# Optimization experiments

Measured on AMD Instinct MI355X. Metric: run time of the kernel, lower is better.

The kernel has to match this reference:

```python
import jax, jax.numpy as jnp
import numpy as np

B, T, D, H = 2, 2048, 1024, 16
HD = D // H  # head_dim = 64


def setup_inputs() -> dict:
    key = jax.random.key(0)
    ks = jax.random.split(key, 6)
    x = jax.random.normal(ks[0], (B, T, D), dtype=jnp.float32)
    wq = jax.random.normal(ks[1], (D, D), dtype=jnp.float32) * (D ** -0.5)
    wk = jax.random.normal(ks[2], (D, D), dtype=jnp.float32) * (D ** -0.5)
    wv = jax.random.normal(ks[3], (D, D), dtype=jnp.float32) * (D ** -0.5)
    wo = jax.random.normal(ks[4], (D, D), dtype=jnp.float32) * (D ** -0.5)
    # RoPE tables: standard inverse-frequency angles, shape [T, head_dim]
    inv_freq = 1.0 / (10000.0 ** (jnp.arange(0, HD, 2, dtype=jnp.float32) / HD))
    ang = jnp.arange(T, dtype=jnp.float32)[:, None] * inv_freq[None, :]  # [T, HD/2]
    ang = jnp.concatenate([ang, ang], axis=-1)  # [T, HD]
    cos, sin = jnp.cos(ang), jnp.sin(ang)
    # causal mask [1,1,T,T]: True where attention is allowed
    mask = jnp.tril(jnp.ones((T, T), dtype=bool))[None, None]
    return {"x": x, "wq": wq, "wk": wk, "wv": wv, "wo": wo,
            "cos": cos, "sin": sin, "mask": mask}


def rotate_half(u):
    u1, u2 = jnp.split(u, 2, axis=-1)
    return jnp.concatenate([-u2, u1], axis=-1)


def reference(x, wq, wk, wv, wo, cos, sin, mask):
    b, t, c = x.shape
    # projections (nn.Linear: y = x @ W^T), reshape to [B, H, T, HD]
    def proj(w):
        return (x @ w.T).reshape(b, t, H, HD).transpose(0, 2, 1, 3)
    q, k, v = proj(wq), proj(wk), proj(wv)
    # inline RoPE: cos/sin broadcast [1,1,T,HD]
    co = cos[:t][None, None]
    si = sin[:t][None, None]
    q = q * co + rotate_half(q) * si
    k = k * co + rotate_half(k) * si
    # scaled dot-product attention with causal mask
    att = jnp.einsum("bhqd,bhkd->bhqk", q, k) * (HD ** -0.5)
    att = jnp.where(mask[:, :, :t, :t], att, -jnp.inf)
    att = jax.nn.softmax(att, axis=-1)
    out = jnp.einsum("bhqk,bhkd->bhqd", att, v)
    out = out.transpose(0, 2, 1, 3).reshape(b, t, c)
    return out @ wo.T
```

## Files before the change

### kernel.cpp

```cpp
#include <hip/hip_runtime.h>
#include <hip/hip_bf16.h>
#include <type_traits>

#define B_  2
#define T_  2048
#define D_  1024
#define H_  16
#define HD_ 64

typedef __attribute__((ext_vector_type(8))) short bf16x8;
typedef __attribute__((ext_vector_type(4))) float f32x4;

__device__ __forceinline__ unsigned short f2b(float x) {
  union { __hip_bfloat16 h; unsigned short u; } c;
  c.h = __float2bfloat16(x);
  return c.u;
}
__device__ __forceinline__ float b2f(unsigned short u) {
  union { unsigned short u; __hip_bfloat16 h; } c;
  c.u = u;
  return __bfloat162float(c.h);
}

__device__ __forceinline__ void ld_g2l_16(const unsigned short* g, unsigned short* l) {
  auto gp = (const __attribute__((address_space(1))) unsigned int*)g;
  auto lp = (__attribute__((address_space(3))) unsigned int*)l;
  __builtin_amdgcn_global_load_lds(gp, lp, 16, 0, 0);
}

__global__ void __launch_bounds__(256)
cast_all(const float* __restrict__ x, const float* __restrict__ wq,
         const float* __restrict__ wk, const float* __restrict__ wv,
         const float* __restrict__ wo, unsigned short* __restrict__ xb,
         unsigned short* __restrict__ wp) {
  int blk = blockIdx.x;
  const float* src;
  unsigned short* dst;
  size_t off;
  if (blk < 2048) {
    src = x; dst = xb; off = (size_t)blk * 2048;
  } else {
    int t = (blk - 2048) >> 9;
    int r = (blk - 2048) & 511;
    src = (t == 0) ? wq : (t == 1) ? wk : (t == 2) ? wv : wo;
    dst = wp + (size_t)t * 1048576;
    off = (size_t)r * 2048;
  }
  size_t i = off + threadIdx.x * 8;
  float4 a = *(const float4*)(src + i);
  float4 b = *(const float4*)(src + i + 4);
  unsigned short h[8] = {f2b(a.x), f2b(a.y), f2b(a.z), f2b(a.w),
                         f2b(b.x), f2b(b.y), f2b(b.z), f2b(b.w)};
  *(uint4*)(dst + i) = *(uint4*)h;
}

template <typename OutT, int MROWS>
__device__ __forceinline__ void gemm_core(const unsigned short* __restrict__ A,
                                          const unsigned short* __restrict__ Bw,
                                          OutT* __restrict__ C, int K, int Ldc) {
  constexpr int MT = MROWS / 32;
  __shared__ unsigned short a_s[MROWS * 32];
  __shared__ unsigned short b_s[128 * 32];
  const int tid = threadIdx.x;
  const int lane = tid & 63;
  const int w = tid >> 6;
  const int m16 = lane & 15;
  const int quad = lane >> 4;
  const int wm = w >> 1, wn = w & 1;
  const int rl = lane >> 2;
  const int cl = (lane & 3) * 8;

  f32x4 acc[MT][4];
#pragma unroll
  for (int i = 0; i < MT; i++)
#pragma unroll
    for (int j = 0; j < 4; j++) acc[i][j] = (f32x4){0.f, 0.f, 0.f, 0.f};

  for (int k0 = 0; k0 < K; k0 += 32) {
#pragma unroll
    for (int t = 0; t < MROWS / 64; t++) {
      int seg = w * 16 + t * 64;
      ld_g2l_16(A + (size_t)(seg + rl) * K + k0 + cl, &a_s[seg * 32]);
    }
#pragma unroll
    for (int j = 0; j < 2; j++) {
      int seg = w * 32 + j * 16;
      ld_g2l_16(Bw + (size_t)(seg + rl) * K + k0 + cl, &b_s[seg * 32]);
    }
    __syncthreads();
    bf16x8 af[MT], bfr[4];
#pragma unroll
    for (int mt = 0; mt < MT; mt++)
      af[mt] = *(const bf16x8*)&a_s[(wm * (MT * 16) + mt * 16 + m16) * 32 + quad * 8];
#pragma unroll
    for (int nt = 0; nt < 4; nt++)
      bfr[nt] = *(const bf16x8*)&b_s[(wn * 64 + nt * 16 + m16) * 32 + quad * 8];
#pragma unroll
    for (int mt = 0; mt < MT; mt++)
#pragma unroll
      for (int nt = 0; nt < 4; nt++)
        acc[mt][nt] = __builtin_amdgcn_mfma_f32_16x16x32_bf16(af[mt], bfr[nt], acc[mt][nt], 0, 0, 0);
    __syncthreads();
  }
#pragma unroll
  for (int mt = 0; mt < MT; mt++)
#pragma unroll
    for (int nt = 0; nt < 4; nt++)
#pragma unroll
      for (int reg = 0; reg < 4; reg++) {
        OutT* p = C + (size_t)(wm * (MT * 16) + mt * 16 + quad * 4 + reg) * Ldc + wn * 64 + nt * 16 + m16;
        if constexpr (std::is_same_v<OutT, float>) *p = acc[mt][nt][reg];
        else *p = f2b(acc[mt][nt][reg]);
      }
}

__global__ void __launch_bounds__(256)
gemm_qkv(const unsigned short* __restrict__ xb, const unsigned short* __restrict__ wp,
         unsigned short* __restrict__ qkv) {
  const int nb = blockIdx.x;
  const int bm = blockIdx.y * 128;
  const int mi = nb >> 3;
  const int bn = (nb & 7) * 128;
  gemm_core<unsigned short, 128>(xb + (size_t)bm * D_,
                                 wp + (size_t)(mi * 1024 + bn) * D_,
                                 qkv + (size_t)mi * (4096ull * D_) + (size_t)bm * D_ + bn,
                                 D_, D_);
}

__global__ void __launch_bounds__(256)
gemm_out(const unsigned short* __restrict__ Ab, const unsigned short* __restrict__ wob,
         float* __restrict__ C) {
  const int bn = blockIdx.x * 128;
  const int bm = blockIdx.y * 64;
  gemm_core<float, 64>(Ab + (size_t)bm * D_, wob + (size_t)bn * D_,
                       C + (size_t)bm * D_ + bn, D_, D_);
}

__global__ void __launch_bounds__(256)
rope_kernel(unsigned short* __restrict__ Q, unsigned short* __restrict__ Kp,
            const float* __restrict__ cosT, const float* __restrict__ sinT) {
  int i = blockIdx.x * 256 + threadIdx.x;
  int d = i & (HD_ - 1);
  int t = (i >> 10) & (T_ - 1);
  float c = cosT[t * HD_ + d];
  float s = sinT[t * HD_ + d];
  float q = b2f(Q[i]), k = b2f(Kp[i]);
  float qp = __shfl_xor(q, 32, 64);
  float kp = __shfl_xor(k, 32, 64);
  float sgn = (d < 32) ? -1.f : 1.f;
  Q[i] = f2b(fmaf(sgn * qp, s, q * c) * 0.125f);
  Kp[i] = f2b(fmaf(sgn * kp, s, k * c));
}

__global__ void __launch_bounds__(512, 4)
attn_kernel(const unsigned short* __restrict__ Q, const unsigned short* __restrict__ K,
            const unsigned short* __restrict__ V, unsigned short* __restrict__ O) {
  __shared__ __align__(16) unsigned short qp_s[128][72];
  __shared__ __align__(16) unsigned short k_s[64][72];
  __shared__ __align__(16) unsigned short vt_s[64][72];

  const int tid = threadIdx.x;
  const int lane = tid & 63;
  const int w = tid >> 6;
  const int m16 = lane & 15;
  const int quad = lane >> 4;

  int x = blockIdx.x;
  int bh, qb;
  if (x < 256) { bh = x >> 4; qb = x & 15; }
  else         { bh = 16 + ((x - 256) >> 4); qb = 15 - ((x - 256) & 15); }
  const int b = bh >> 4, h = bh & 15;
  const int q0 = qb * 128;

  const unsigned short* Qb = Q + ((size_t)b * T_ + q0) * D_ + h * HD_;
  const unsigned short* Kb = K + (size_t)b * T_ * D_ + h * HD_;
  const unsigned short* Vb = V + (size_t)b * T_ * D_ + h * HD_;

#pragma unroll
  for (int i = 0; i < 2; i++) {
    int idx = tid + i * 512;
    int r = idx >> 3, c = idx & 7;
    *(bf16x8*)&qp_s[r][c * 8] = *(const bf16x8*)(Qb + (size_t)r * D_ + c * 8);
  }
  __syncthreads();
  bf16x8 q_frag[2];
  q_frag[0] = *(const bf16x8*)&qp_s[w * 16 + m16][quad * 8];
  q_frag[1] = *(const bf16x8*)&qp_s[w * 16 + m16][32 + quad * 8];

  f32x4 o_acc[4];
#pragma unroll
  for (int dt = 0; dt < 4; dt++) o_acc[dt] = (f32x4){0.f, 0.f, 0.f, 0.f};
  float m_i = -1e30f, l_i = 0.f;
  const int rg = q0 + w * 16 + m16;
  const int rmax = q0 + w * 16 + 15;
  const int ktmax = (q0 + 127) >> 6;

  for (int kt = 0; kt <= ktmax; kt++) {
    {
      int r = tid >> 3, c = tid & 7;
      const unsigned short* Kt = Kb + (size_t)(kt * 64 + r) * D_ + c * 8;
      const unsigned short* Vt = Vb + (size_t)(kt * 64 + r) * D_ + c * 8;
      *(bf16x8*)&k_s[r][c * 8] = *(const bf16x8*)Kt;
      bf16x8 vv = *(const bf16x8*)Vt;
      int jb = r >> 3, jl = r & 7;
#pragma unroll
      for (int e = 0; e < 8; e++) {
        int d = c * 8 + e;
        vt_s[d][((jb ^ (d >> 3)) << 3) | jl] = ((const unsigned short*)&vv)[e];
      }
    }
    __syncthreads();

    if (kt * 64 <= rmax) {
      f32x4 sf[4];
#pragma unroll
      for (int jt = 0; jt < 4; jt++) {
        bf16x8 a0 = *(const bf16x8*)&k_s[jt * 16 + m16][quad * 8];
        bf16x8 a1 = *(const bf16x8*)&k_s[jt * 16 + m16][32 + quad * 8];
        f32x4 acc = (f32x4){0.f, 0.f, 0.f, 0.f};
        acc = __builtin_amdgcn_mfma_f32_16x16x32_bf16(a0, q_frag[0], acc, 0, 0, 0);
        acc = __builtin_amdgcn_mfma_f32_16x16x32_bf16(a1, q_frag[1], acc, 0, 0, 0);
        sf[jt] = acc;
      }
      if (kt * 64 + 63 > q0 + w * 16) {
#pragma unroll
        for (int jt = 0; jt < 4; jt++)
#pragma unroll
          for (int reg = 0; reg < 4; reg++) {
            int jg = kt * 64 + jt * 16 + quad * 4 + reg;
            if (jg > rg) sf[jt][reg] = -1e30f;
          }
      }
      float mx = sf[0][0];
#pragma unroll
      for (int jt = 0; jt < 4; jt++)
#pragma unroll
        for (int reg = 0; reg < 4; reg++) mx = fmaxf(mx, sf[jt][reg]);
      mx = fmaxf(mx, __shfl_xor(mx, 16, 64));
      mx = fmaxf(mx, __shfl_xor(mx, 32, 64));
      float mn = fmaxf(m_i, mx);
      float alpha = __expf(m_i - mn);
      float lt = 0.f;
      float p[4][4];
#pragma unroll
      for (int jt = 0; jt < 4; jt++)
#pragma unroll
        for (int reg = 0; reg < 4; reg++) {
          p[jt][reg] = __expf(sf[jt][reg] - mn);
          lt += p[jt][reg];
        }
      lt += __shfl_xor(lt, 16, 64);
      lt += __shfl_xor(lt, 32, 64);
      l_i = l_i * alpha + lt;
      m_i = mn;
#pragma unroll
      for (int dt = 0; dt < 4; dt++)
#pragma unroll
        for (int reg = 0; reg < 4; reg++) o_acc[dt][reg] *= alpha;
#pragma unroll
      for (int jt = 0; jt < 4; jt++) {
        unsigned short pk[4] = {f2b(p[jt][0]), f2b(p[jt][1]), f2b(p[jt][2]), f2b(p[jt][3])};
        *(uint2*)&qp_s[w * 16 + m16][jt * 16 + quad * 4] = *(uint2*)pk;
      }
      bf16x8 bp0 = *(const bf16x8*)&qp_s[w * 16 + m16][quad * 8];
      bf16x8 bp1 = *(const bf16x8*)&qp_s[w * 16 + m16][32 + quad * 8];
#pragma unroll
      for (int dt = 0; dt < 4; dt++) {
        int rowd = dt * 16 + m16;
        bf16x8 a0 = *(const bf16x8*)&vt_s[rowd][((quad ^ (rowd >> 3)) << 3)];
        bf16x8 a1 = *(const bf16x8*)&vt_s[rowd][(((4 + quad) ^ (rowd >> 3)) << 3)];
        o_acc[dt] = __builtin_amdgcn_mfma_f32_16x16x32_bf16(a0, bp0, o_acc[dt], 0, 0, 0);
        o_acc[dt] = __builtin_amdgcn_mfma_f32_16x16x32_bf16(a1, bp1, o_acc[dt], 0, 0, 0);
      }
    }
    __syncthreads();
  }

  float inv = 1.f / l_i;
#pragma unroll
  for (int dt = 0; dt < 4; dt++) {
    unsigned short ok[4];
#pragma unroll
    for (int reg = 0; reg < 4; reg++) ok[reg] = f2b(o_acc[dt][reg] * inv);
    *(uint2*)&qp_s[w * 16 + m16][dt * 16 + quad * 4] = *(uint2*)ok;
  }
  __syncthreads();
  unsigned short* Ob = O + ((size_t)b * T_ + q0) * D_ + h * HD_;
#pragma unroll
  for (int i = 0; i < 2; i++) {
    int idx = tid + i * 512;
    int r = idx >> 3, c = idx & 7;
    *(bf16x8*)(Ob + (size_t)r * D_ + c * 8) = *(const bf16x8*)&qp_s[r][c * 8];
  }
}

extern "C" void kernel_launch(void* const* d_in, const int* in_sizes, int n_in,
                              void* d_out, int out_size, void* d_ws, size_t ws_size,
                              hipStream_t stream) {
  const float* x    = (const float*)d_in[0];
  const float* wq   = (const float*)d_in[1];
  const float* wk   = (const float*)d_in[2];
  const float* wv   = (const float*)d_in[3];
  const float* wo   = (const float*)d_in[4];
  const float* cosT = (const float*)d_in[5];
  const float* sinT = (const float*)d_in[6];
  float* out = (float*)d_out;

  const size_t NTOK = (size_t)B_ * T_;
  const size_t SZ   = NTOK * D_;
  unsigned short* xb   = (unsigned short*)d_ws;
  unsigned short* Wp   = xb + SZ;
  unsigned short* QKVh = Wp + 4 * 1048576;
  unsigned short* Ab   = QKVh + 3 * SZ;

  cast_all<<<4096, 256, 0, stream>>>(x, wq, wk, wv, wo, xb, Wp);
  gemm_qkv<<<dim3(24, 32), 256, 0, stream>>>(xb, Wp, QKVh);
  rope_kernel<<<(int)(SZ / 256), 256, 0, stream>>>(QKVh, QKVh + SZ, cosT, sinT);
  attn_kernel<<<512, 512, 0, stream>>>(QKVh, QKVh + SZ, QKVh + 2 * SZ, Ab);
  gemm_out<<<dim3(8, 64), 256, 0, stream>>>(Ab, Wp + 3 * 1048576, out);
}
```

Before: 220.5 us.

## Fuse RoPE into QKV GEMM, double-buffer GEMM and attention K/V, pre-transpose V

Result: faster. 208.3 us (-5.5%).

```diff
diff --git a/kernel.cpp b/kernel.cpp
--- a/kernel.cpp
+++ b/kernel.cpp
@@ -57,10 +57,12 @@
 template <typename OutT, int MROWS>
 __device__ __forceinline__ void gemm_core(const unsigned short* __restrict__ A,
                                           const unsigned short* __restrict__ Bw,
-                                          OutT* __restrict__ C, int K, int Ldc) {
+                                          OutT* __restrict__ C, int K, int Ldc,
+                                          int rope_mode, const float* __restrict__ cosT,
+                                          const float* __restrict__ sinT, int tok0) {
   constexpr int MT = MROWS / 32;
-  __shared__ unsigned short a_s[MROWS * 32];
-  __shared__ unsigned short b_s[128 * 32];
+  __shared__ unsigned short a_s[2][MROWS * 32];
+  __shared__ unsigned short b_s[2][128 * 32];
   const int tid = threadIdx.x;
   const int lane = tid & 63;
   const int w = tid >> 6;
@@ -76,31 +78,58 @@
 #pragma unroll
     for (int j = 0; j < 4; j++) acc[i][j] = (f32x4){0.f, 0.f, 0.f, 0.f};
 
-  for (int k0 = 0; k0 < K; k0 += 32) {
+  auto stage = [&](int it, int bs) {
+    int k0 = it * 32;
 #pragma unroll
     for (int t = 0; t < MROWS / 64; t++) {
       int seg = w * 16 + t * 64;
-      ld_g2l_16(A + (size_t)(seg + rl) * K + k0 + cl, &a_s[seg * 32]);
+      ld_g2l_16(A + (size_t)(seg + rl) * K + k0 + cl, &a_s[bs][seg * 32]);
     }
 #pragma unroll
-    for (int j = 0; j < 2; j++) {
-      int seg = w * 32 + j * 16;
-      ld_g2l_16(Bw + (size_t)(seg + rl) * K + k0 + cl, &b_s[seg * 32]);
+    for (int j2 = 0; j2 < 2; j2++) {
+      int seg = w * 32 + j2 * 16;
+      ld_g2l_16(Bw + (size_t)(seg + rl) * K + k0 + cl, &b_s[bs][seg * 32]);
     }
-    __syncthreads();
+  };
+
+  const int nit = K / 32;
+  stage(0, 0);
+  __syncthreads();
+  for (int it = 0; it < nit; it++) {
+    int cur = it & 1;
+    if (it + 1 < nit) stage(it + 1, cur ^ 1);
     bf16x8 af[MT], bfr[4];
 #pragma unroll
     for (int mt = 0; mt < MT; mt++)
-      af[mt] = *(const bf16x8*)&a_s[(wm * (MT * 16) + mt * 16 + m16) * 32 + quad * 8];
+      af[mt] = *(const bf16x8*)&a_s[cur][(wm * (MT * 16) + mt * 16 + m16) * 32 + quad * 8];
 #pragma unroll
     for (int nt = 0; nt < 4; nt++)
-      bfr[nt] = *(const bf16x8*)&b_s[(wn * 64 + nt * 16 + m16) * 32 + quad * 8];
+      bfr[nt] = *(const bf16x8*)&b_s[cur][(wn * 64 + nt * 16 + m16) * 32 + quad * 8];
 #pragma unroll
     for (int mt = 0; mt < MT; mt++)
 #pragma unroll
       for (int nt = 0; nt < 4; nt++)
         acc[mt][nt] = __builtin_amdgcn_mfma_f32_16x16x32_bf16(af[mt], bfr[nt], acc[mt][nt], 0, 0, 0);
     __syncthreads();
+  }
+
+  if (rope_mode) {
+    float scale = (rope_mode == 2) ? 0.125f : 1.f;
+#pragma unroll
+    for (int mt = 0; mt < MT; mt++)
+#pragma unroll
+      for (int reg = 0; reg < 4; reg++) {
+        int t = (tok0 + wm * (MT * 16) + mt * 16 + quad * 4 + reg) & (T_ - 1);
+#pragma unroll
+        for (int nt = 0; nt < 2; nt++) {
+          int d = nt * 16 + m16;
+          float co = cosT[t * HD_ + d] * scale;
+          float si = sinT[t * HD_ + d] * scale;
+          float lo = acc[mt][nt][reg], hi = acc[mt][nt + 2][reg];
+          acc[mt][nt][reg]     = lo * co - hi * si;
+          acc[mt][nt + 2][reg] = hi * co + lo * si;
+        }
+      }
   }
 #pragma unroll
   for (int mt = 0; mt < MT; mt++)
@@ -116,15 +145,17 @@
 
 __global__ void __launch_bounds__(256)
 gemm_qkv(const unsigned short* __restrict__ xb, const unsigned short* __restrict__ wp,
-         unsigned short* __restrict__ qkv) {
+         unsigned short* __restrict__ qkv, const float* __restrict__ cosT,
+         const float* __restrict__ sinT) {
   const int nb = blockIdx.x;
   const int bm = blockIdx.y * 128;
   const int mi = nb >> 3;
   const int bn = (nb & 7) * 128;
+  const int rope_mode = (mi == 0) ? 2 : (mi == 1) ? 1 : 0;
   gemm_core<unsigned short, 128>(xb + (size_t)bm * D_,
                                  wp + (size_t)(mi * 1024 + bn) * D_,
                                  qkv + (size_t)mi * (4096ull * D_) + (size_t)bm * D_ + bn,
-                                 D_, D_);
+                                 D_, D_, rope_mode, cosT, sinT, bm);
 }
 
 __global__ void __launch_bounds__(256)
@@ -133,37 +164,44 @@
   const int bn = blockIdx.x * 128;
   const int bm = blockIdx.y * 64;
   gemm_core<float, 64>(Ab + (size_t)bm * D_, wob + (size_t)bn * D_,
-                       C + (size_t)bm * D_ + bn, D_, D_);
+                       C + (size_t)bm * D_ + bn, D_, D_, 0, nullptr, nullptr, 0);
 }
 
 __global__ void __launch_bounds__(256)
-rope_kernel(unsigned short* __restrict__ Q, unsigned short* __restrict__ Kp,
-            const float* __restrict__ cosT, const float* __restrict__ sinT) {
-  int i = blockIdx.x * 256 + threadIdx.x;
-  int d = i & (HD_ - 1);
-  int t = (i >> 10) & (T_ - 1);
-  float c = cosT[t * HD_ + d];
-  float s = sinT[t * HD_ + d];
-  float q = b2f(Q[i]), k = b2f(Kp[i]);
-  float qp = __shfl_xor(q, 32, 64);
-  float kp = __shfl_xor(k, 32, 64);
-  float sgn = (d < 32) ? -1.f : 1.f;
-  Q[i] = f2b(fmaf(sgn * qp, s, q * c) * 0.125f);
-  Kp[i] = f2b(fmaf(sgn * kp, s, k * c));
+vtrans(const unsigned short* __restrict__ V, unsigned short* __restrict__ VT) {
+  __shared__ unsigned short tile[64][72];
+  const int tid = threadIdx.x;
+  const int tb = blockIdx.x, h = blockIdx.y, b = blockIdx.z;
+  const unsigned short* Vb = V + ((size_t)b * T_ + tb * 64) * D_ + h * HD_;
+  int r = tid >> 2;
+  int c = (tid & 3) * 16;
+  bf16x8 v0 = *(const bf16x8*)(Vb + (size_t)r * D_ + c);
+  bf16x8 v1 = *(const bf16x8*)(Vb + (size_t)r * D_ + c + 8);
+#pragma unroll
+  for (int e = 0; e < 8; e++) tile[c + e][r] = ((unsigned short*)&v0)[e];
+#pragma unroll
+  for (int e = 0; e < 8; e++) tile[c + 8 + e][r] = ((unsigned short*)&v1)[e];
+  __syncthreads();
+  unsigned short* VTb = VT + ((size_t)b * H_ + h) * HD_ * T_ + tb * 64;
+  *(bf16x8*)(VTb + (size_t)r * T_ + c)     = *(const bf16x8*)&tile[r][c];
+  *(bf16x8*)(VTb + (size_t)r * T_ + c + 8) = *(const bf16x8*)&tile[r][c + 8];
 }
 
 __global__ void __launch_bounds__(512, 4)
 attn_kernel(const unsigned short* __restrict__ Q, const unsigned short* __restrict__ K,
-            const unsigned short* __restrict__ V, unsigned short* __restrict__ O) {
+            const unsigned short* __restrict__ VT, unsigned short* __restrict__ O) {
   __shared__ __align__(16) unsigned short qp_s[128][72];
-  __shared__ __align__(16) unsigned short k_s[64][72];
-  __shared__ __align__(16) unsigned short vt_s[64][72];
+  __shared__ __align__(16) unsigned short k_s[2][64 * 64];
+  __shared__ __align__(16) unsigned short vt_s[2][64 * 64];
 
   const int tid = threadIdx.x;
   const int lane = tid & 63;
   const int w = tid >> 6;
   const int m16 = lane & 15;
   const int quad = lane >> 4;
+  const int swz = m16 & 7;
+  const int pc0 = quad ^ swz;
+  const int pc1 = pc0 ^ 4;
 
   int x = blockIdx.x;
   int bh, qb;
@@ -174,7 +212,7 @@
 
   const unsigned short* Qb = Q + ((size_t)b * T_ + q0) * D_ + h * HD_;
   const unsigned short* Kb = K + (size_t)b * T_ * D_ + h * HD_;
-  const unsigned short* Vb = V + (size_t)b * T_ * D_ + h * HD_;
+  const unsigned short* VTb = VT + ((size_t)b * H_ + h) * HD_ * T_;
 
 #pragma unroll
   for (int i = 0; i < 2; i++) {
@@ -182,10 +220,14 @@
     int r = idx >> 3, c = idx & 7;
     *(bf16x8*)&qp_s[r][c * 8] = *(const bf16x8*)(Qb + (size_t)r * D_ + c * 8);
   }
-  __syncthreads();
-  bf16x8 q_frag[2];
-  q_frag[0] = *(const bf16x8*)&qp_s[w * 16 + m16][quad * 8];
-  q_frag[1] = *(const bf16x8*)&qp_s[w * 16 + m16][32 + quad * 8];
+
+  auto stage_kv = [&](int kt, int bs) {
+    int r_sub = lane >> 3, c = lane & 7;
+    int cs = (c ^ r_sub) * 8;
+    int gr = w * 8 + r_sub;
+    ld_g2l_16(Kb + (size_t)(kt * 64 + gr) * D_ + cs, &k_s[bs][w * 8 * 64]);
+    ld_g2l_16(VTb + (size_t)gr * T_ + kt * 64 + cs, &vt_s[bs][w * 8 * 64]);
+  };
 
   f32x4 o_acc[4];
 #pragma unroll
@@ -195,28 +237,24 @@
   const int rmax = q0 + w * 16 + 15;
   const int ktmax = (q0 + 127) >> 6;
 
+  stage_kv(0, 0);
+  __syncthreads();
+  bf16x8 q_frag[2];
+  q_frag[0] = *(const bf16x8*)&qp_s[w * 16 + m16][quad * 8];
+  q_frag[1] = *(const bf16x8*)&qp_s[w * 16 + m16][32 + quad * 8];
+
   for (int kt = 0; kt <= ktmax; kt++) {
-    {
-      int r = tid >> 3, c = tid & 7;
-      const unsigned short* Kt = Kb + (size_t)(kt * 64 + r) * D_ + c * 8;
-      const unsigned short* Vt = Vb + (size_t)(kt * 64 + r) * D_ + c * 8;
-      *(bf16x8*)&k_s[r][c * 8] = *(const bf16x8*)Kt;
-      bf16x8 vv = *(const bf16x8*)Vt;
-      int jb = r >> 3, jl = r & 7;
-#pragma unroll
-      for (int e = 0; e < 8; e++) {
-        int d = c * 8 + e;
-        vt_s[d][((jb ^ (d >> 3)) << 3) | jl] = ((const unsigned short*)&vv)[e];
-      }
-    }
-    __syncthreads();
+    int cur = kt & 1;
+    if (kt < ktmax) stage_kv(kt + 1, cur ^ 1);
 
     if (kt * 64 <= rmax) {
+      const unsigned short* kc = &k_s[cur][0];
+      const unsigned short* vc = &vt_s[cur][0];
       f32x4 sf[4];
 #pragma unroll
       for (int jt = 0; jt < 4; jt++) {
-        bf16x8 a0 = *(const bf16x8*)&k_s[jt * 16 + m16][quad * 8];
-        bf16x8 a1 = *(const bf16x8*)&k_s[jt * 16 + m16][32 + quad * 8];
+        bf16x8 a0 = *(const bf16x8*)&kc[(jt * 16 + m16) * 64 + pc0 * 8];
+        bf16x8 a1 = *(const bf16x8*)&kc[(jt * 16 + m16) * 64 + pc1 * 8];
         f32x4 acc = (f32x4){0.f, 0.f, 0.f, 0.f};
         acc = __builtin_amdgcn_mfma_f32_16x16x32_bf16(a0, q_frag[0], acc, 0, 0, 0);
         acc = __builtin_amdgcn_mfma_f32_16x16x32_bf16(a1, q_frag[1], acc, 0, 0, 0);
@@ -267,8 +305,8 @@
 #pragma unroll
       for (int dt = 0; dt < 4; dt++) {
         int rowd = dt * 16 + m16;
-        bf16x8 a0 = *(const bf16x8*)&vt_s[rowd][((quad ^ (rowd >> 3)) << 3)];
-        bf16x8 a1 = *(const bf16x8*)&vt_s[rowd][(((4 + quad) ^ (rowd >> 3)) << 3)];
+        bf16x8 a0 = *(const bf16x8*)&vc[rowd * 64 + pc0 * 8];
+        bf16x8 a1 = *(const bf16x8*)&vc[rowd * 64 + pc1 * 8];
         o_acc[dt] = __builtin_amdgcn_mfma_f32_16x16x32_bf16(a0, bp0, o_acc[dt], 0, 0, 0);
         o_acc[dt] = __builtin_amdgcn_mfma_f32_16x16x32_bf16(a1, bp1, o_acc[dt], 0, 0, 0);
       }
@@ -312,10 +350,11 @@
   unsigned short* Wp   = xb + SZ;
   unsigned short* QKVh = Wp + 4 * 1048576;
   unsigned short* Ab   = QKVh + 3 * SZ;
+  unsigned short* VTb  = xb;
 
   cast_all<<<4096, 256, 0, stream>>>(x, wq, wk, wv, wo, xb, Wp);
-  gemm_qkv<<<dim3(24, 32), 256, 0, stream>>>(xb, Wp, QKVh);
-  rope_kernel<<<(int)(SZ / 256), 256, 0, stream>>>(QKVh, QKVh + SZ, cosT, sinT);
-  attn_kernel<<<512, 512, 0, stream>>>(QKVh, QKVh + SZ, QKVh + 2 * SZ, Ab);
+  gemm_qkv<<<dim3(24, 32), 256, 0, stream>>>(xb, Wp, QKVh, cosT, sinT);
+  vtrans<<<dim3(32, 16, 2), 256, 0, stream>>>(QKVh + 2 * SZ, VTb);
+  attn_kernel<<<512, 512, 0, stream>>>(QKVh, QKVh + SZ, VTb, Ab);
   gemm_out<<<dim3(8, 64), 256, 0, stream>>>(Ab, Wp + 3 * 1048576, out);
 }
```
